# Performance work log

Measured on AMD Instinct MI355X. Metric: run time of the kernel, lower is better.

Reference implementation:

```python
import jax, jax.numpy as jnp
import numpy as np


def _maxpool2x2(t):
    # t: [B, C, H, W] -> [B, C, H//2, W//2]
    b, c, h, w = t.shape
    return t.reshape(b, c, h // 2, 2, w // 2, 2).max(axis=(3, 5))


def setup_inputs() -> dict:
    key = jax.random.key(0)
    ks = jax.random.split(key, 6)
    B, C, H, W = 16, 64, 64, 64
    x = jax.random.normal(ks[0], (B, C, H, W), dtype=jnp.float32)
    # 1x1 conv weights (no bias), stored as [out_ch, in_ch]
    s = 0.05
    W_theta = jax.random.normal(ks[1], (C // 8, C), dtype=jnp.float32) * s
    W_phi = jax.random.normal(ks[2], (C // 8, C), dtype=jnp.float32) * s
    W_g = jax.random.normal(ks[3], (C // 2, C), dtype=jnp.float32) * s
    W_attn = jax.random.normal(ks[4], (C, C // 2), dtype=jnp.float32) * s
    sigma = jnp.ones((1,), dtype=jnp.float32) * 0.5  # nonzero so attn path matters
    return {"x": x, "W_theta": W_theta, "W_phi": W_phi, "W_g": W_g,
            "W_attn": W_attn, "sigma": sigma}


def reference(x, W_theta, W_phi, W_g, W_attn, sigma):
    B, C, H, W = x.shape
    N = H * W
    M = N // 4
    # 1x1 convs are channel matmuls
    theta = jnp.einsum('oc,bchw->bohw', W_theta, x).reshape(B, C // 8, N)      # [B, C/8, N]
    phi = _maxpool2x2(jnp.einsum('oc,bchw->bohw', W_phi, x)).reshape(B, C // 8, M)  # [B, C/8, M]
    attn = jax.nn.softmax(jnp.einsum('bkn,bkm->bnm', theta, phi), axis=-1)    # [B, N, M]
    g = _maxpool2x2(jnp.einsum('oc,bchw->bohw', W_g, x)).reshape(B, C // 2, M)  # [B, C/2, M]
    attn_g = jnp.einsum('bgm,bnm->bgn', g, attn).reshape(B, C // 2, H, W)      # [B, C/2, H, W]
    attn_g = jnp.einsum('oc,bchw->bohw', W_attn, attn_g)                        # [B, C, H, W]
    return x + sigma * attn_g
```

## Files before the change

### kernel.cpp

```cpp
#include <hip/hip_runtime.h>
#include <hip/hip_bf16.h>

#define CC 64
#define NN 4096
#define MM 1024

typedef __attribute__((ext_vector_type(4))) short s4b;
typedef __attribute__((ext_vector_type(8))) short s8b;
typedef __attribute__((ext_vector_type(4))) float float4v;

__device__ inline unsigned short f2bf(float f) {
    union { float f; unsigned u; } v; v.f = f;
    unsigned r = v.u + 0x7fff + ((v.u >> 16) & 1);
    return (unsigned short)(r >> 16);
}

__device__ inline float4v mfma16(s4b a, s4b b, float4v c) {
#if __has_builtin(__builtin_amdgcn_mfma_f32_16x16x16bf16_1k)
    return __builtin_amdgcn_mfma_f32_16x16x16bf16_1k(a, b, c, 0, 0, 0);
#else
    float4v d;
    asm volatile("v_mfma_f32_16x16x16_bf16 %0, %1, %2, %3"
                 : "=v"(d) : "v"(a), "v"(b), "v"(c));
    return d;
#endif
}

__device__ inline float4v mfma32(s8b a, s8b b, float4v c) {
#if __has_builtin(__builtin_amdgcn_mfma_f32_16x16x32_bf16)
    return __builtin_amdgcn_mfma_f32_16x16x32_bf16(a, b, c, 0, 0, 0);
#else
    float4v d;
    asm volatile("v_mfma_f32_16x16x32_bf16 %0, %1, %2, %3"
                 : "=v"(d) : "v"(a), "v"(b), "v"(c));
    return d;
#endif
}

__global__ __launch_bounds__(256) void prep_kernel(
    const float* __restrict__ x,
    const float* __restrict__ Wth,
    const float* __restrict__ Wph,
    const float* __restrict__ Wg,
    unsigned short* __restrict__ thT,
    unsigned short* __restrict__ phiP,
    unsigned short* __restrict__ gP)
{
    __shared__ __align__(16) float wtg[4 * 776];
    __shared__ __align__(16) float pbuf[32 * 40];

    const int tid  = threadIdx.x;
    const int b    = blockIdx.y;
    const int hp   = blockIdx.x;
    const int lane = tid & 63;
    const int w    = tid >> 6;
    const int h2   = lane >> 4;
    const int sl   = lane & 15;
    const int row  = w >> 1;
    const int cp   = (w & 1) * 16 + sl;

    for (int idx = tid; idx < 3072; idx += 256) {
        const int c = idx / 48, j = idx % 48;
        float v;
        if (j < 8)       v = Wth[j * 64 + c];
        else if (j < 16) v = Wph[(j - 8) * 64 + c];
        else             v = Wg[(j - 16) * 64 + c];
        wtg[(c >> 4) * 776 + (c & 15) * 48 + j] = v;
    }
    __syncthreads();

    const int n = (2 * hp + row) * 64 + 2 * cp;
    const float* xb = x + (size_t)b * CC * NN + (size_t)(h2 * 16) * NN + n;

    float2 xv[16];
#pragma unroll
    for (int u = 0; u < 16; ++u) xv[u] = *(const float2*)&xb[(size_t)u * NN];

    float ax[48], ay[48];
#pragma unroll
    for (int j = 0; j < 48; ++j) { ax[j] = 0.f; ay[j] = 0.f; }

    const float* wr0 = &wtg[h2 * 776];
#pragma unroll
    for (int u = 0; u < 16; ++u) {
        const float* wrow = wr0 + u * 48;
        const float2 xu = xv[u];
#pragma unroll
        for (int j = 0; j < 48; ++j) {
            const float wv_ = wrow[j];
            ax[j] = fmaf(wv_, xu.x, ax[j]);
            ay[j] = fmaf(wv_, xu.y, ay[j]);
        }
    }

#pragma unroll
    for (int j = 0; j < 48; ++j) {
        ax[j] += __shfl_xor(ax[j], 16, 64);
        ay[j] += __shfl_xor(ay[j], 16, 64);
        ax[j] += __shfl_xor(ax[j], 32, 64);
        ay[j] += __shfl_xor(ay[j], 32, 64);
    }

    if (h2 == 0) {
        union { unsigned short s[16]; uint4 v[2]; } pk;
#pragma unroll
        for (int j = 0; j < 8; ++j) {
            pk.s[j]     = f2bf(ax[j] * 1.44269504f);
            pk.s[8 + j] = f2bf(ay[j] * 1.44269504f);
        }
        uint4* dst = (uint4*)&thT[((size_t)b * NN + n) * 8];
        dst[0] = pk.v[0]; dst[1] = pk.v[1];
    }

    float hm[40];
#pragma unroll
    for (int j = 0; j < 40; ++j) hm[j] = fmaxf(ax[8 + j], ay[8 + j]);

    if (row == 1 && h2 == 1) {
#pragma unroll
        for (int j4 = 0; j4 < 10; ++j4) {
            float4 t;
            t.x = hm[j4 * 4 + 0]; t.y = hm[j4 * 4 + 1];
            t.z = hm[j4 * 4 + 2]; t.w = hm[j4 * 4 + 3];
            *(float4*)&pbuf[cp * 40 + j4 * 4] = t;
        }
    }
    __syncthreads();

    if (row == 0 && h2 >= 2) {
        const int m = hp * 32 + cp;
        if (h2 == 2) {
            union { unsigned short s[8]; uint4 v; } pk;
#pragma unroll
            for (int j = 0; j < 8; ++j)
                pk.s[j] = f2bf(fmaxf(hm[j], pbuf[cp * 40 + j]));
            *(uint4*)&phiP[((size_t)b * MM + m) * 8] = pk.v;
#pragma unroll
            for (int j = 8; j < 24; ++j)
                gP[((size_t)b * 32 + (j - 8)) * MM + m] =
                    f2bf(fmaxf(hm[j], pbuf[cp * 40 + j]));
        } else {
#pragma unroll
            for (int j = 24; j < 40; ++j)
                gP[((size_t)b * 32 + (j - 8)) * MM + m] =
                    f2bf(fmaxf(hm[j], pbuf[cp * 40 + j]));
        }
    }
}

__global__ __launch_bounds__(256) void attn_mfma(
    const unsigned short* __restrict__ thT,
    const unsigned short* __restrict__ phiP,
    const unsigned short* __restrict__ gP,
    const float* __restrict__ x,
    const float* __restrict__ Wa,
    const float* __restrict__ sigma,
    float* __restrict__ out)
{
    constexpr int GP = 264;
    constexpr int OBP = 40;

    __shared__ __align__(16) union {
        struct {
            unsigned short phi[256 * 8 + 16];
            unsigned short g[32 * GP];
        } m;
        unsigned short obb[128 * OBP];
    } sh;

    const int tid  = threadIdx.x;
    const int lane = tid & 63;
    const int wv   = tid >> 6;
    const int c15  = lane & 15;
    const int quad = lane >> 4;
    const int b    = blockIdx.y;
    const int n0   = blockIdx.x * 128;

    union { unsigned short s[8]; s8b v; } wfrag;
    {
        const float* wr = Wa + (wv * 16 + c15) * 32 + quad * 8;
        const float4 w0 = *(const float4*)wr;
        const float4 w1 = *(const float4*)(wr + 4);
        wfrag.s[0] = f2bf(w0.x); wfrag.s[1] = f2bf(w0.y);
        wfrag.s[2] = f2bf(w0.z); wfrag.s[3] = f2bf(w0.w);
        wfrag.s[4] = f2bf(w1.x); wfrag.s[5] = f2bf(w1.y);
        wfrag.s[6] = f2bf(w1.z); wfrag.s[7] = f2bf(w1.w);
    }

    s4b zero4 = {0, 0, 0, 0};
    s4b bthA = zero4, bthB = zero4;
    if (quad < 2) {
        union { uint2 u; s4b s; } t;
        t.u = *(const uint2*)&thT[((size_t)b * NN + n0 + wv * 32 + c15) * 8 + quad * 4];
        bthA = t.s;
        t.u = *(const uint2*)&thT[((size_t)b * NN + n0 + wv * 32 + 16 + c15) * 8 + quad * 4];
        bthB = t.s;
    }

    float4v accA0 = {0.f, 0.f, 0.f, 0.f};
    float4v accA1 = {0.f, 0.f, 0.f, 0.f};
    float4v accB0 = {0.f, 0.f, 0.f, 0.f};
    float4v accB1 = {0.f, 0.f, 0.f, 0.f};
    float zaccA = 0.f, zaccB = 0.f;

    for (int ch = 0; ch < 4; ++ch) {
        __syncthreads();
        {
            const int r  = tid & 7;
            const int q3 = (tid >> 3) & 3;
            const int slot = (tid & ~31) | ((r >> 2) << 4) | (q3 << 2) | (r & 3);
            *(uint4*)&sh.m.phi[slot * 8] =
                *(const uint4*)&phiP[((size_t)b * MM + ch * 256 + tid) * 8];
            if (tid < 2) {
                uint4 z4; z4.x = z4.y = z4.z = z4.w = 0u;
                *(uint4*)&sh.m.phi[256 * 8 + tid * 8] = z4;
            }
        }
#pragma unroll
        for (int it = 0; it < 4; ++it) {
            const int idx = tid + 256 * it;
            const int grow = idx >> 5, c32 = idx & 31;
            *(uint4*)&sh.m.g[grow * GP + c32 * 8] =
                *(const uint4*)&gP[((size_t)b * 32 + grow) * MM + ch * 256 + c32 * 8];
        }
        __syncthreads();

        const unsigned short* pA  = &sh.m.phi[c15 * 8 + quad * 4];
        const unsigned short* pg0 = &sh.m.g[c15 * GP + quad * 8];
        const unsigned short* pg1 = pg0 + 16 * GP;

#pragma unroll
        for (int g32 = 0; g32 < 8; ++g32) {
            union { uint2 u; s4b s; } apA, apB;
            apA.u = *(const uint2*)&pA[g32 * 256];
            apB.u = *(const uint2*)&pA[g32 * 256 + 128];

            float4v cz = {0.f, 0.f, 0.f, 0.f};
            float4v sAlo = mfma16(apA.s, bthA, cz);
            float4v sAhi = mfma16(apB.s, bthA, cz);
            float4v sBlo = mfma16(apA.s, bthB, cz);
            float4v sBhi = mfma16(apB.s, bthB, cz);

            union { float f; unsigned u; } a0, a1, a2, a3, b0, b1, b2, b3;
            a0.f = __builtin_amdgcn_exp2f(sAlo[0]);
            a1.f = __builtin_amdgcn_exp2f(sAlo[1]);
            a2.f = __builtin_amdgcn_exp2f(sAlo[2]);
            a3.f = __builtin_amdgcn_exp2f(sAlo[3]);
            b0.f = __builtin_amdgcn_exp2f(sAhi[0]);
            b1.f = __builtin_amdgcn_exp2f(sAhi[1]);
            b2.f = __builtin_amdgcn_exp2f(sAhi[2]);
            b3.f = __builtin_amdgcn_exp2f(sAhi[3]);
            zaccA += ((a0.f + a1.f) + (a2.f + a3.f)) +
                     ((b0.f + b1.f) + (b2.f + b3.f));
            union { uint4 u; s8b s; } paA;
            paA.u.x = __builtin_amdgcn_perm(a1.u, a0.u, 0x07060302u);
            paA.u.y = __builtin_amdgcn_perm(a3.u, a2.u, 0x07060302u);
            paA.u.z = __builtin_amdgcn_perm(b1.u, b0.u, 0x07060302u);
            paA.u.w = __builtin_amdgcn_perm(b3.u, b2.u, 0x07060302u);

            a0.f = __builtin_amdgcn_exp2f(sBlo[0]);
            a1.f = __builtin_amdgcn_exp2f(sBlo[1]);
            a2.f = __builtin_amdgcn_exp2f(sBlo[2]);
            a3.f = __builtin_amdgcn_exp2f(sBlo[3]);
            b0.f = __builtin_amdgcn_exp2f(sBhi[0]);
            b1.f = __builtin_amdgcn_exp2f(sBhi[1]);
            b2.f = __builtin_amdgcn_exp2f(sBhi[2]);
            b3.f = __builtin_amdgcn_exp2f(sBhi[3]);
            zaccB += ((a0.f + a1.f) + (a2.f + a3.f)) +
                     ((b0.f + b1.f) + (b2.f + b3.f));
            union { uint4 u; s8b s; } paB;
            paB.u.x = __builtin_amdgcn_perm(a1.u, a0.u, 0x07060302u);
            paB.u.y = __builtin_amdgcn_perm(a3.u, a2.u, 0x07060302u);
            paB.u.z = __builtin_amdgcn_perm(b1.u, b0.u, 0x07060302u);
            paB.u.w = __builtin_amdgcn_perm(b3.u, b2.u, 0x07060302u);

            union { uint4 u; s8b s; } bg0, bg1;
            bg0.u = *(const uint4*)&pg0[g32 * 32];
            bg1.u = *(const uint4*)&pg1[g32 * 32];

            accA0 = mfma32(paA.s, bg0.s, accA0);
            accA1 = mfma32(paA.s, bg1.s, accA1);
            accB0 = mfma32(paB.s, bg0.s, accB0);
            accB1 = mfma32(paB.s, bg1.s, accB1);
        }
    }

    float zA = zaccA, zB = zaccB;
    zA += __shfl_xor(zA, 16, 64);
    zA += __shfl_xor(zA, 32, 64);
    zB += __shfl_xor(zB, 16, 64);
    zB += __shfl_xor(zB, 32, 64);
    const float rzqA = __builtin_amdgcn_rcpf(zA);
    const float rzqB = __builtin_amdgcn_rcpf(zB);

    __syncthreads();

#pragma unroll
    for (int r = 0; r < 4; ++r) {
        const float rzA = __shfl(rzqA, quad * 4 + r, 64);
        const float rzB = __shfl(rzqB, quad * 4 + r, 64);
        const int qlA = wv * 32 + quad * 4 + r;
        const int qlB = qlA + 16;
        sh.obb[qlA * OBP + c15]      = f2bf(accA0[r] * rzA);
        sh.obb[qlA * OBP + 16 + c15] = f2bf(accA1[r] * rzA);
        sh.obb[qlB * OBP + c15]      = f2bf(accB0[r] * rzB);
        sh.obb[qlB * OBP + 16 + c15] = f2bf(accB1[r] * rzB);
    }
    __syncthreads();

    const float sg = sigma[0];
#pragma unroll
    for (int t = 0; t < 8; ++t) {
        union { uint4 u; s8b s; } bo;
        bo.u = *(const uint4*)&sh.obb[(t * 16 + c15) * OBP + quad * 8];
        float4v cz = {0.f, 0.f, 0.f, 0.f};
        float4v oc = mfma32(wfrag.v, bo.s, cz);
#pragma unroll
        for (int r = 0; r < 4; ++r) {
            const size_t oi = ((size_t)b * CC + wv * 16 + quad * 4 + r) * NN
                              + n0 + t * 16 + c15;
            out[oi] = x[oi] + sg * oc[r];
        }
    }
}

extern "C" void kernel_launch(void* const* d_in, const int* in_sizes, int n_in,
                              void* d_out, int out_size, void* d_ws, size_t ws_size,
                              hipStream_t stream) {
    const float* x      = (const float*)d_in[0];
    const float* W_th   = (const float*)d_in[1];
    const float* W_ph   = (const float*)d_in[2];
    const float* W_g    = (const float*)d_in[3];
    const float* W_attn = (const float*)d_in[4];
    const float* sigma  = (const float*)d_in[5];
    float* out = (float*)d_out;

    const int B = 16;
    unsigned short* thT  = (unsigned short*)d_ws;
    unsigned short* phiP = thT + (size_t)B * NN * 8;
    unsigned short* gP   = phiP + (size_t)B * MM * 8;

    prep_kernel<<<dim3(32, 16), 256, 0, stream>>>(x, W_th, W_ph, W_g,
                                                  thT, phiP, gP);
    attn_mfma<<<dim3(32, 16), 256, 0, stream>>>(thT, phiP, gP, x,
                                                W_attn, sigma, out);
}
```

Measured before the change: 106.2 us.

## Split attention key range across two wave groups and restructure prep projection

The attention kernel now launches 512 threads per block: two groups of four waves each process half of the M key dimension, staging their own phi/g tiles, then combine partial accumulators and softmax denominators through shared memory before normalisation and the output projection. This doubles the number of waves working on the same query tile, aiming to hide MFMA/exp latency with more parallelism per block. The prep kernel is rewritten so each thread owns one pixel and half the channels, reducing via shared memory instead of cross-lane shuffles, with pooling done by a separate shared-memory pass. The change costs extra shared memory, an added reduction step, and less coalesced scalar stores in prep.

```diff
diff --git a/kernel.cpp b/kernel.cpp
--- a/kernel.cpp
+++ b/kernel.cpp
@@ -46,109 +46,76 @@
     unsigned short* __restrict__ phiP,
     unsigned short* __restrict__ gP)
 {
-    __shared__ __align__(16) float wtg[4 * 776];
-    __shared__ __align__(16) float pbuf[32 * 40];
+    __shared__ float wt[64 * 48];
+    __shared__ float buf[128 * 49];
 
     const int tid  = threadIdx.x;
     const int b    = blockIdx.y;
     const int hp   = blockIdx.x;
-    const int lane = tid & 63;
-    const int w    = tid >> 6;
-    const int h2   = lane >> 4;
-    const int sl   = lane & 15;
-    const int row  = w >> 1;
-    const int cp   = (w & 1) * 16 + sl;
-
-    for (int idx = tid; idx < 3072; idx += 256) {
+    const int pix  = tid & 127;
+    const int half = tid >> 7;
+
+    for (int idx = tid; idx < 64 * 48; idx += 256) {
         const int c = idx / 48, j = idx % 48;
         float v;
         if (j < 8)       v = Wth[j * 64 + c];
         else if (j < 16) v = Wph[(j - 8) * 64 + c];
         else             v = Wg[(j - 16) * 64 + c];
-        wtg[(c >> 4) * 776 + (c & 15) * 48 + j] = v;
-    }
-    __syncthreads();
-
-    const int n = (2 * hp + row) * 64 + 2 * cp;
-    const float* xb = x + (size_t)b * CC * NN + (size_t)(h2 * 16) * NN + n;
-
-    float2 xv[16];
-#pragma unroll
-    for (int u = 0; u < 16; ++u) xv[u] = *(const float2*)&xb[(size_t)u * NN];
-
-    float ax[48], ay[48];
-#pragma unroll
-    for (int j = 0; j < 48; ++j) { ax[j] = 0.f; ay[j] = 0.f; }
-
-    const float* wr0 = &wtg[h2 * 776];
-#pragma unroll
-    for (int u = 0; u < 16; ++u) {
-        const float* wrow = wr0 + u * 48;
-        const float2 xu = xv[u];
-#pragma unroll
-        for (int j = 0; j < 48; ++j) {
-            const float wv_ = wrow[j];
-            ax[j] = fmaf(wv_, xu.x, ax[j]);
-            ay[j] = fmaf(wv_, xu.y, ay[j]);
-        }
-    }
-
-#pragma unroll
-    for (int j = 0; j < 48; ++j) {
-        ax[j] += __shfl_xor(ax[j], 16, 64);
-        ay[j] += __shfl_xor(ay[j], 16, 64);
-        ax[j] += __shfl_xor(ax[j], 32, 64);
-        ay[j] += __shfl_xor(ay[j], 32, 64);
-    }
-
-    if (h2 == 0) {
-        union { unsigned short s[16]; uint4 v[2]; } pk;
-#pragma unroll
-        for (int j = 0; j < 8; ++j) {
-            pk.s[j]     = f2bf(ax[j] * 1.44269504f);
-            pk.s[8 + j] = f2bf(ay[j] * 1.44269504f);
-        }
-        uint4* dst = (uint4*)&thT[((size_t)b * NN + n) * 8];
-        dst[0] = pk.v[0]; dst[1] = pk.v[1];
-    }
-
-    float hm[40];
-#pragma unroll
-    for (int j = 0; j < 40; ++j) hm[j] = fmaxf(ax[8 + j], ay[8 + j]);
-
-    if (row == 1 && h2 == 1) {
-#pragma unroll
-        for (int j4 = 0; j4 < 10; ++j4) {
-            float4 t;
-            t.x = hm[j4 * 4 + 0]; t.y = hm[j4 * 4 + 1];
-            t.z = hm[j4 * 4 + 2]; t.w = hm[j4 * 4 + 3];
-            *(float4*)&pbuf[cp * 40 + j4 * 4] = t;
-        }
-    }
-    __syncthreads();
-
-    if (row == 0 && h2 >= 2) {
-        const int m = hp * 32 + cp;
-        if (h2 == 2) {
-            union { unsigned short s[8]; uint4 v; } pk;
-#pragma unroll
-            for (int j = 0; j < 8; ++j)
-                pk.s[j] = f2bf(fmaxf(hm[j], pbuf[cp * 40 + j]));
-            *(uint4*)&phiP[((size_t)b * MM + m) * 8] = pk.v;
-#pragma unroll
-            for (int j = 8; j < 24; ++j)
-                gP[((size_t)b * 32 + (j - 8)) * MM + m] =
-                    f2bf(fmaxf(hm[j], pbuf[cp * 40 + j]));
-        } else {
-#pragma unroll
-            for (int j = 24; j < 40; ++j)
-                gP[((size_t)b * 32 + (j - 8)) * MM + m] =
-                    f2bf(fmaxf(hm[j], pbuf[cp * 40 + j]));
-        }
-    }
-}
-
-__global__ __launch_bounds__(256) void attn_mfma(
+        wt[c * 48 + j] = v;
+    }
+    __syncthreads();
+
+    const int n = (2 * hp + (pix >> 6)) * 64 + (pix & 63);
+    const float* xb = x + (size_t)b * CC * NN + (size_t)half * 32 * NN + n;
+
+    float acc[48];
+#pragma unroll
+    for (int j = 0; j < 48; ++j) acc[j] = 0.f;
+
+#pragma unroll
+    for (int c0 = 0; c0 < 32; c0 += 16) {
+        float xv[16];
+#pragma unroll
+        for (int u = 0; u < 16; ++u) xv[u] = xb[(size_t)(c0 + u) * NN];
+#pragma unroll
+        for (int u = 0; u < 16; ++u) {
+            const float* wrow = &wt[(half * 32 + c0 + u) * 48];
+#pragma unroll
+            for (int j = 0; j < 48; ++j) acc[j] += wrow[j] * xv[u];
+        }
+    }
+
+    if (half == 1) {
+#pragma unroll
+        for (int j = 0; j < 48; ++j) buf[pix * 49 + j] = acc[j];
+    }
+    __syncthreads();
+
+    if (half == 0) {
+#pragma unroll
+        for (int j = 0; j < 48; ++j) acc[j] += buf[pix * 49 + j];
+        union { unsigned short s[8]; uint4 v; } pk;
+#pragma unroll
+        for (int j = 0; j < 8; ++j) pk.s[j] = f2bf(acc[j] * 1.44269504f);
+        *(uint4*)&thT[((size_t)b * NN + n) * 8] = pk.v;
+#pragma unroll
+        for (int j = 0; j < 40; ++j) buf[pix * 49 + j] = acc[8 + j];
+    }
+    __syncthreads();
+
+    for (int idx = tid; idx < 1280; idx += 256) {
+        const int pm = idx & 31;
+        const int j  = idx >> 5;
+        const int p00 = 2 * pm, p10 = 64 + 2 * pm;
+        const float v = fmaxf(fmaxf(buf[p00 * 49 + j], buf[(p00 + 1) * 49 + j]),
+                              fmaxf(buf[p10 * 49 + j], buf[(p10 + 1) * 49 + j]));
+        const int m = hp * 32 + pm;
+        if (j < 8) phiP[((size_t)b * MM + m) * 8 + j] = f2bf(v);
+        else       gP[((size_t)b * 32 + (j - 8)) * MM + m] = f2bf(v);
+    }
+}
+
+__global__ __launch_bounds__(512, 4) void attn_mfma(
     const unsigned short* __restrict__ thT,
     const unsigned short* __restrict__ phiP,
     const unsigned short* __restrict__ gP,
@@ -157,20 +124,26 @@
     const float* __restrict__ sigma,
     float* __restrict__ out)
 {
-    constexpr int GP = 264;
-    constexpr int OBP = 40;
+    constexpr int GP     = 264;
+    constexpr int OBP    = 40;
+    constexpr int PHI_SH = 256 * 8 + 16;
 
     __shared__ __align__(16) union {
         struct {
-            unsigned short phi[256 * 8 + 16];
-            unsigned short g[32 * GP];
-        } m;
-        unsigned short obb[128 * OBP];
+            unsigned short phi[2][PHI_SH];
+            unsigned short g[2][32 * GP];
+        } st;
+        struct {
+            float part[72][64];
+            unsigned short obb[128 * OBP];
+        } cb;
     } sh;
 
     const int tid  = threadIdx.x;
     const int lane = tid & 63;
     const int wv   = tid >> 6;
+    const int wq   = wv & 3;
+    const int wk   = wv >> 2;
     const int c15  = lane & 15;
     const int quad = lane >> 4;
     const int b    = blockIdx.y;
@@ -178,7 +151,7 @@
 
     union { unsigned short s[8]; s8b v; } wfrag;
     {
-        const float* wr = Wa + (wv * 16 + c15) * 32 + quad * 8;
+        const float* wr = Wa + (wq * 16 + c15) * 32 + quad * 8;
         const float4 w0 = *(const float4*)wr;
         const float4 w1 = *(const float4*)(wr + 4);
         wfrag.s[0] = f2bf(w0.x); wfrag.s[1] = f2bf(w0.y);
@@ -191,9 +164,9 @@
     s4b bthA = zero4, bthB = zero4;
     if (quad < 2) {
         union { uint2 u; s4b s; } t;
-        t.u = *(const uint2*)&thT[((size_t)b * NN + n0 + wv * 32 + c15) * 8 + quad * 4];
+        t.u = *(const uint2*)&thT[((size_t)b * NN + n0 + wq * 32 + c15) * 8 + quad * 4];
         bthA = t.s;
-        t.u = *(const uint2*)&thT[((size_t)b * NN + n0 + wv * 32 + 16 + c15) * 8 + quad * 4];
+        t.u = *(const uint2*)&thT[((size_t)b * NN + n0 + wq * 32 + 16 + c15) * 8 + quad * 4];
         bthB = t.s;
     }
 
@@ -203,31 +176,33 @@
     float4v accB1 = {0.f, 0.f, 0.f, 0.f};
     float zaccA = 0.f, zaccB = 0.f;
 
-    for (int ch = 0; ch < 4; ++ch) {
+    const unsigned short* pA  = &sh.st.phi[wk][c15 * 8 + quad * 4];
+    const unsigned short* pg0 = &sh.st.g[wk][c15 * GP + quad * 8];
+    const unsigned short* pg1 = pg0 + 16 * GP;
+
+    for (int ci = 0; ci < 2; ++ci) {
         __syncthreads();
         {
-            const int r  = tid & 7;
-            const int q3 = (tid >> 3) & 3;
-            const int slot = (tid & ~31) | ((r >> 2) << 4) | (q3 << 2) | (r & 3);
-            *(uint4*)&sh.m.phi[slot * 8] =
-                *(const uint4*)&phiP[((size_t)b * MM + ch * 256 + tid) * 8];
-            if (tid < 2) {
+            const int s = tid >> 8, k = tid & 255;
+            const int r = k & 7, q3 = (k >> 3) & 3;
+            const int slot = (k & ~31) | ((r >> 2) << 4) | (q3 << 2) | (r & 3);
+            *(uint4*)&sh.st.phi[s][slot * 8] =
+                *(const uint4*)&phiP[((size_t)b * MM + s * 512 + ci * 256 + k) * 8];
+            if (tid < 4) {
                 uint4 z4; z4.x = z4.y = z4.z = z4.w = 0u;
-                *(uint4*)&sh.m.phi[256 * 8 + tid * 8] = z4;
+                *(uint4*)&sh.st.phi[tid >> 1][2048 + (tid & 1) * 8] = z4;
             }
         }
 #pragma unroll
         for (int it = 0; it < 4; ++it) {
-            const int idx = tid + 256 * it;
-            const int grow = idx >> 5, c32 = idx & 31;
-            *(uint4*)&sh.m.g[grow * GP + c32 * 8] =
-                *(const uint4*)&gP[((size_t)b * 32 + grow) * MM + ch * 256 + c32 * 8];
+            const int idx  = tid + 512 * it;
+            const int s    = idx >> 10;
+            const int rc   = idx & 1023;
+            const int grow = rc >> 5, c32 = rc & 31;
+            *(uint4*)&sh.st.g[s][grow * GP + c32 * 8] =
+                *(const uint4*)&gP[((size_t)b * 32 + grow) * MM + s * 512 + ci * 256 + c32 * 8];
         }
         __syncthreads();
-
-        const unsigned short* pA  = &sh.m.phi[c15 * 8 + quad * 4];
-        const unsigned short* pg0 = &sh.m.g[c15 * GP + quad * 8];
-        const unsigned short* pg1 = pg0 + 16 * GP;
 
 #pragma unroll
         for (int g32 = 0; g32 < 8; ++g32) {
@@ -285,39 +260,65 @@
         }
     }
 
-    float zA = zaccA, zB = zaccB;
-    zA += __shfl_xor(zA, 16, 64);
-    zA += __shfl_xor(zA, 32, 64);
-    zB += __shfl_xor(zB, 16, 64);
-    zB += __shfl_xor(zB, 32, 64);
-    const float rzqA = __builtin_amdgcn_rcpf(zA);
-    const float rzqB = __builtin_amdgcn_rcpf(zB);
-
-    __syncthreads();
-
-#pragma unroll
-    for (int r = 0; r < 4; ++r) {
-        const float rzA = __shfl(rzqA, quad * 4 + r, 64);
-        const float rzB = __shfl(rzqB, quad * 4 + r, 64);
-        const int qlA = wv * 32 + quad * 4 + r;
-        const int qlB = qlA + 16;
-        sh.obb[qlA * OBP + c15]      = f2bf(accA0[r] * rzA);
-        sh.obb[qlA * OBP + 16 + c15] = f2bf(accA1[r] * rzA);
-        sh.obb[qlB * OBP + c15]      = f2bf(accB0[r] * rzB);
-        sh.obb[qlB * OBP + 16 + c15] = f2bf(accB1[r] * rzB);
+    __syncthreads();
+    if (wk == 1) {
+#pragma unroll
+        for (int r = 0; r < 4; ++r) {
+            sh.cb.part[     r * 4 + wq][lane] = accA0[r];
+            sh.cb.part[16 + r * 4 + wq][lane] = accA1[r];
+            sh.cb.part[32 + r * 4 + wq][lane] = accB0[r];
+            sh.cb.part[48 + r * 4 + wq][lane] = accB1[r];
+        }
+        sh.cb.part[64 + wq][lane] = zaccA;
+        sh.cb.part[68 + wq][lane] = zaccB;
+    }
+    __syncthreads();
+
+    if (wk == 0) {
+#pragma unroll
+        for (int r = 0; r < 4; ++r) {
+            accA0[r] += sh.cb.part[     r * 4 + wq][lane];
+            accA1[r] += sh.cb.part[16 + r * 4 + wq][lane];
+            accB0[r] += sh.cb.part[32 + r * 4 + wq][lane];
+            accB1[r] += sh.cb.part[48 + r * 4 + wq][lane];
+        }
+        zaccA += sh.cb.part[64 + wq][lane];
+        zaccB += sh.cb.part[68 + wq][lane];
+
+        float zA = zaccA, zB = zaccB;
+        zA += __shfl_xor(zA, 16, 64);
+        zA += __shfl_xor(zA, 32, 64);
+        zB += __shfl_xor(zB, 16, 64);
+        zB += __shfl_xor(zB, 32, 64);
+        const float rzqA = __builtin_amdgcn_rcpf(zA);
+        const float rzqB = __builtin_amdgcn_rcpf(zB);
+
+#pragma unroll
+        for (int r = 0; r < 4; ++r) {
+            const float rzA = __shfl(rzqA, quad * 4 + r, 64);
+            const float rzB = __shfl(rzqB, quad * 4 + r, 64);
+            const int qlA = wq * 32 + quad * 4 + r;
+            const int qlB = qlA + 16;
+            sh.cb.obb[qlA * OBP + c15]      = f2bf(accA0[r] * rzA);
+            sh.cb.obb[qlA * OBP + 16 + c15] = f2bf(accA1[r] * rzA);
+            sh.cb.obb[qlB * OBP + c15]      = f2bf(accB0[r] * rzB);
+            sh.cb.obb[qlB * OBP + 16 + c15] = f2bf(accB1[r] * rzB);
+        }
     }
     __syncthreads();
 
     const float sg = sigma[0];
-#pragma unroll
-    for (int t = 0; t < 8; ++t) {
+    const int ow = wv & 3, qh = wv >> 2;
+#pragma unroll
+    for (int tt = 0; tt < 4; ++tt) {
+        const int t = qh * 4 + tt;
         union { uint4 u; s8b s; } bo;
-        bo.u = *(const uint4*)&sh.obb[(t * 16 + c15) * OBP + quad * 8];
+        bo.u = *(const uint4*)&sh.cb.obb[(t * 16 + c15) * OBP + quad * 8];
         float4v cz = {0.f, 0.f, 0.f, 0.f};
         float4v oc = mfma32(wfrag.v, bo.s, cz);
 #pragma unroll
         for (int r = 0; r < 4; ++r) {
-            const size_t oi = ((size_t)b * CC + wv * 16 + quad * 4 + r) * NN
+            const size_t oi = ((size_t)b * CC + ow * 16 + quad * 4 + r) * NN
                               + n0 + t * 16 + c15;
             out[oi] = x[oi] + sg * oc[r];
         }
@@ -342,6 +343,6 @@
 
     prep_kernel<<<dim3(32, 16), 256, 0, stream>>>(x, W_th, W_ph, W_g,
                                                   thT, phiP, gP);
-    attn_mfma<<<dim3(32, 16), 256, 0, stream>>>(thT, phiP, gP, x,
+    attn_mfma<<<dim3(32, 16), 512, 0, stream>>>(thT, phiP, gP, x,
                                                 W_attn, sigma, out);
 }
```

Measured after the change: 140.8 us. +32.6%, slower.
